# Optimization experiments

Measured on AMD Instinct MI355X. Metric: run time of the kernel, lower is better.

Reference implementation:

```python
import jax, jax.numpy as jnp
import numpy as np
import math

PS = 16            # patch size for SigmaPredictor
HID = 8            # hidden_dim
SCALE = HID ** -0.5
SIGMA_CAP = 6.0    # BoundedSoftplus threshold
EPS_S = 1e-6       # BoundedSoftplus eps


def setup_inputs() -> dict:
    key = jax.random.key(0)
    ks = jax.random.split(key, 10)
    B, C, H, W = 2, 1, 384, 384
    d_in = C * PS * PS  # 256
    r = lambda k_, sh: jax.random.normal(k_, sh, dtype=jnp.float32) * 0.1
    z = lambda sh: jnp.zeros(sh, dtype=jnp.float32)
    return {
        "x": jax.random.uniform(ks[0], (B, C, H, W), dtype=jnp.float32),
        "Wq": r(ks[1], (d_in, HID)), "bq": z((HID,)),
        "Wk": r(ks[2], (d_in, HID)), "bk": z((HID,)),
        "Wv": r(ks[3], (d_in, HID)), "bv": z((HID,)),
        "Wsq": r(ks[4], (HID, HID)), "bsq": z((HID,)),
        "Wsk": r(ks[5], (HID, HID)), "bsk": z((HID,)),
        "Wsv": r(ks[6], (HID, HID)), "bsv": z((HID,)),
        "ln_g": jnp.ones((HID,), jnp.float32), "ln_b": z((HID,)),
        "Wp": r(ks[7], (HID, 3)),
        # bias ~4 -> sigmas ~4 -> kernel size k=13 (production-scale support)
        "bp": jnp.full((3,), 4.0, dtype=jnp.float32),
    }


def _attn(q, k, v):
    a = jax.nn.softmax(jnp.einsum('bnd,bmd->bnm', q, k) * SCALE, axis=-1)
    return jnp.einsum('bnm,bmd->bnd', a, v)


def _predict_sigmas(x, Wq, bq, Wk, bk, Wv, bv, Wsq, bsq, Wsk, bsk, Wsv, bsv, ln_g, ln_b, Wp, bp):
    b, c, h, w = x.shape
    Hp, Wn = h // PS, w // PS
    # unfold into non-overlapping patches: [B, Hp*Wn, C*PS*PS]
    pat = x.reshape(b, c, Hp, PS, Wn, PS).transpose(0, 2, 4, 1, 3, 5).reshape(b, Hp * Wn, c * PS * PS)
    feats = _attn(pat @ Wq + bq, pat @ Wk + bk, pat @ Wv + bv)
    o = _attn(feats @ Wsq + bsq, feats @ Wsk + bsk, feats @ Wsv + bsv)
    mu = o.mean(-1, keepdims=True)
    var = ((o - mu) ** 2).mean(-1, keepdims=True)
    o = (o - mu) / jnp.sqrt(var + 1e-5) * ln_g + ln_b
    s = jnp.minimum(jax.nn.softplus(o @ Wp + bp), SIGMA_CAP) + EPS_S  # BoundedSoftplus
    s = s.reshape(b, Hp, Wn, 3)
    # nearest-neighbor upsample to full resolution: [B, H, W, 3]
    return jnp.repeat(jnp.repeat(s, PS, axis=1), PS, axis=2)


def _bilateral(x, s, k):
    b, c, h, w = x.shape
    sx, sy, sr = s[..., 0], s[..., 1], s[..., 2]
    half = k // 2
    xp = jnp.pad(x, ((0, 0), (0, 0), (half, half), (half, half)))
    # [B, C, H, W, k*k], dy-major to match torch unfold/meshgrid ordering
    patches = jnp.stack([xp[:, :, dy:dy + h, dx:dx + w]
                         for dy in range(k) for dx in range(k)], axis=-1)
    coords = jnp.arange(-half, half + 1, dtype=jnp.float32)
    yy, xx = jnp.meshgrid(coords, coords, indexing='ij')
    xx2 = (xx ** 2).reshape(-1)
    yy2 = (yy ** 2).reshape(-1)
    # spatial kernel [B, H, W, k*k]
    sp = jnp.exp(-xx2 / (2 * sx[..., None] ** 2) - yy2 / (2 * sy[..., None] ** 2))
    # range kernel (C == 1 branch) [B, C, H, W, k*k]
    rg = jnp.exp(-(x[..., None] - patches) ** 2 / (2 * sr[:, None, :, :, None] ** 2))
    comb = sp[:, None] * rg
    norm = comb / (comb.sum(-1, keepdims=True) + 1e-8)
    return (patches * norm).sum(-1)


def reference(x, Wq, bq, Wk, bk, Wv, bv, Wsq, bsq, Wsk, bsk, Wsv, bsv, ln_g, ln_b, Wp, bp):
    s = _predict_sigmas(x, Wq, bq, Wk, bk, Wv, bv, Wsq, bsq, Wsk, bsk, Wsv, bsv, ln_g, ln_b, Wp, bp)
    # data-dependent kernel size, computed eagerly (matches torch .item())
    m = float(jnp.maximum(s[..., 0].max(), s[..., 1].max()))
    k = int(2 * math.ceil(m + 1))
    if k % 2 == 0:
        k += 1
    return _bilateral(x, s, k)
```

## Files before the change

### kernel.cpp

```cpp
#include <hip/hip_runtime.h>

#define N_TOK 576
#define HP    24
#define PS    16
#define IMG   384
#define ATTN_SCALE 0.35355339059327373f

__global__ __launch_bounds__(256) void k_qkv1(
    const float* __restrict__ x,
    const float* __restrict__ Wq, const float* __restrict__ bq,
    const float* __restrict__ Wk, const float* __restrict__ bk,
    const float* __restrict__ Wv, const float* __restrict__ bv,
    float* __restrict__ q1, float* __restrict__ k1, float* __restrict__ v1,
    int* __restrict__ smax)
{
    const int blk = blockIdx.x;
    const int b  = blk / N_TOK;
    const int n  = blk % N_TOK;
    const int py = n / HP, px = n % HP;
    const int t  = threadIdx.x;
    const int iy = t >> 4, ix = t & 15;

    if (blk == 0 && t == 0) smax[0] = 0;

    const float pv = x[b*IMG*IMG + (py*PS + iy)*IMG + (px*PS + ix)];

    float acc[24];
#pragma unroll
    for (int h = 0; h < 8; ++h) {
        acc[h]      = pv * Wq[t*8 + h];
        acc[8 + h]  = pv * Wk[t*8 + h];
        acc[16 + h] = pv * Wv[t*8 + h];
    }
#pragma unroll
    for (int off = 32; off > 0; off >>= 1) {
#pragma unroll
        for (int j = 0; j < 24; ++j)
            acc[j] += __shfl_down(acc[j], off);
    }
    __shared__ float red[4][24];
    const int lane = t & 63, w = t >> 6;
    if (lane == 0) {
#pragma unroll
        for (int j = 0; j < 24; ++j) red[w][j] = acc[j];
    }
    __syncthreads();
    if (t < 24) {
        float s = red[0][t] + red[1][t] + red[2][t] + red[3][t];
        const int h = t & 7, mat = t >> 3;
        const float* bias = (mat == 0) ? bq : (mat == 1) ? bk : bv;
        float* dst = (mat == 0) ? q1 : (mat == 1) ? k1 : v1;
        dst[(b*N_TOK + n)*8 + h] = s + bias[h];
    }
}

__device__ __forceinline__ void attn_core(
    const float* __restrict__ qp, const float* __restrict__ kb,
    const float* __restrict__ vb, int lane, float f[8], float* ssum_out)
{
    const float4 qa = *(const float4*)(qp);
    const float4 qb_ = *(const float4*)(qp + 4);
    float qv[8] = {qa.x, qa.y, qa.z, qa.w, qb_.x, qb_.y, qb_.z, qb_.w};

    float sc[9], mx = -1e30f;
#pragma unroll
    for (int ch = 0; ch < 9; ++ch) {
        const float* kp = kb + (ch*64 + lane)*8;
        const float4 ka = *(const float4*)(kp);
        const float4 kb2 = *(const float4*)(kp + 4);
        float d = qv[0]*ka.x + qv[1]*ka.y + qv[2]*ka.z + qv[3]*ka.w
                + qv[4]*kb2.x + qv[5]*kb2.y + qv[6]*kb2.z + qv[7]*kb2.w;
        d *= ATTN_SCALE;
        sc[ch] = d;
        mx = fmaxf(mx, d);
    }
#pragma unroll
    for (int off = 32; off > 0; off >>= 1) mx = fmaxf(mx, __shfl_xor(mx, off));

    float ssum = 0.f, o[8];
#pragma unroll
    for (int h = 0; h < 8; ++h) o[h] = 0.f;
#pragma unroll
    for (int ch = 0; ch < 9; ++ch) {
        const float p = __expf(sc[ch] - mx);
        ssum += p;
        const float* vp = vb + (ch*64 + lane)*8;
        const float4 va = *(const float4*)(vp);
        const float4 vb2 = *(const float4*)(vp + 4);
        o[0] += p*va.x;  o[1] += p*va.y;  o[2] += p*va.z;  o[3] += p*va.w;
        o[4] += p*vb2.x; o[5] += p*vb2.y; o[6] += p*vb2.z; o[7] += p*vb2.w;
    }
#pragma unroll
    for (int off = 32; off > 0; off >>= 1) {
        ssum += __shfl_xor(ssum, off);
#pragma unroll
        for (int h = 0; h < 8; ++h) o[h] += __shfl_xor(o[h], off);
    }
    const float inv = 1.f/ssum;
#pragma unroll
    for (int h = 0; h < 8; ++h) f[h] = o[h]*inv;
    *ssum_out = ssum;
}

__global__ __launch_bounds__(256) void k_attn1(
    const float* __restrict__ q1, const float* __restrict__ k1, const float* __restrict__ v1,
    const float* __restrict__ Wsq, const float* __restrict__ bsq,
    const float* __restrict__ Wsk, const float* __restrict__ bsk,
    const float* __restrict__ Wsv, const float* __restrict__ bsv,
    float* __restrict__ q2, float* __restrict__ k2, float* __restrict__ v2)
{
    const int lane = threadIdx.x & 63;
    const int wv   = threadIdx.x >> 6;
    const int tok  = blockIdx.x*4 + wv;
    const int b    = tok / N_TOK;

    float f[8], ssum;
    attn_core(q1 + tok*8, k1 + b*N_TOK*8, v1 + b*N_TOK*8, lane, f, &ssum);

    if (lane < 24) {
        const int mat = lane >> 3, h = lane & 7;
        const float* Wm = (mat==0)?Wsq:(mat==1)?Wsk:Wsv;
        const float* bm = (mat==0)?bsq:(mat==1)?bsk:bsv;
        float s = bm[h];
#pragma unroll
        for (int j = 0; j < 8; ++j) s += f[j]*Wm[j*8 + h];
        float* dst = (mat==0)?q2:(mat==1)?k2:v2;
        dst[tok*8 + h] = s;
    }
}

__global__ __launch_bounds__(256) void k_attn2(
    const float* __restrict__ q2, const float* __restrict__ k2, const float* __restrict__ v2,
    const float* __restrict__ ln_g, const float* __restrict__ ln_b,
    const float* __restrict__ Wp,   const float* __restrict__ bp,
    float* __restrict__ sig, int* __restrict__ smax)
{
    const int lane = threadIdx.x & 63;
    const int wv   = threadIdx.x >> 6;
    const int tok  = blockIdx.x*4 + wv;
    const int b    = tok / N_TOK;

    float f[8], ssum;
    attn_core(q2 + tok*8, k2 + b*N_TOK*8, v2 + b*N_TOK*8, lane, f, &ssum);

    if (lane == 0) {
        float mu = 0.f;
#pragma unroll
        for (int h = 0; h < 8; ++h) mu += f[h];
        mu *= 0.125f;
        float var = 0.f;
#pragma unroll
        for (int h = 0; h < 8; ++h) { const float d = f[h]-mu; var += d*d; }
        var *= 0.125f;
        const float rinv = rsqrtf(var + 1e-5f);
        float on[8];
#pragma unroll
        for (int h = 0; h < 8; ++h)
            on[h] = (f[h]-mu)*rinv*ln_g[h] + ln_b[h];
        float sv[3];
#pragma unroll
        for (int c = 0; c < 3; ++c) {
            float z = bp[c];
#pragma unroll
            for (int j = 0; j < 8; ++j) z += on[j]*Wp[j*3 + c];
            const float sp = (z > 20.f) ? z : log1pf(__expf(z));
            sv[c] = fminf(sp, 6.0f) + 1e-6f;
            sig[tok*3 + c] = sv[c];
        }
        atomicMax(smax, __float_as_int(fmaxf(sv[0], sv[1])));
    }
}

template<int HALF>
__device__ __forceinline__ float bilat_core(
    const float* __restrict__ tile, int tx, int ty,
    float ax, float ay, float ar)
{
    constexpr int K = 2*HALF + 1;
    const float c = tile[(ty+HALF)*40 + (tx+HALF)];

    float ex[K];
#pragma unroll
    for (int d = 0; d < K; ++d) {
        const float fd = (float)(d - HALF);
        ex[d] = ax*fd*fd;
    }

    float num = 0.f, den = 0.f;
#pragma unroll
    for (int dy = 0; dy < K; ++dy) {
        const float fy = (float)(dy - HALF);
        const float ey = ay*fy*fy;
        const float* row = &tile[(ty+dy)*40 + tx];
#pragma unroll
        for (int dx = 0; dx < K; ++dx) {
            const float p = row[dx];
            const float d = c - p;
            const float w = __expf(ey + ex[dx] + ar*d*d);
            den += w;
            num += w*p;
        }
    }
    return num/(den + 1e-8f);
}

__global__ __launch_bounds__(256) void k_bilat(
    const float* __restrict__ x, const float* __restrict__ sig,
    const int* __restrict__ smaxi, float* __restrict__ out)
{
    __shared__ float tile[32*40];
    const int blk = blockIdx.x;
    const int b  = blk / N_TOK;
    const int n  = blk % N_TOK;
    const int py = n / HP, px = n % HP;
    const int tx = threadIdx.x & 15, ty = threadIdx.x >> 4;

    const float m = __int_as_float(smaxi[0]);
    int half = (int)ceilf(m + 1.0f);
    half = (half < 1) ? 1 : (half > 8) ? 8 : half;

    const float sx = sig[blk*3 + 0];
    const float sy = sig[blk*3 + 1];
    const float sr = sig[blk*3 + 2];

    const int tilew = PS + 2*half;
    const float* xb = x + b*IMG*IMG;
    for (int yy = ty; yy < tilew; yy += 16) {
        const int gy = py*PS + yy - half;
        for (int xx = tx; xx < tilew; xx += 16) {
            const int gx = px*PS + xx - half;
            float v = 0.f;
            if ((unsigned)gy < IMG && (unsigned)gx < IMG)
                v = xb[gy*IMG + gx];
            tile[yy*40 + xx] = v;
        }
    }
    __syncthreads();

    const float ax = -0.5f/(sx*sx);
    const float ay = -0.5f/(sy*sy);
    const float ar = -0.5f/(sr*sr);

    float r;
    switch (half) {
        case 1: r = bilat_core<1>(tile, tx, ty, ax, ay, ar); break;
        case 2: r = bilat_core<2>(tile, tx, ty, ax, ay, ar); break;
        case 3: r = bilat_core<3>(tile, tx, ty, ax, ay, ar); break;
        case 4: r = bilat_core<4>(tile, tx, ty, ax, ay, ar); break;
        case 5: r = bilat_core<5>(tile, tx, ty, ax, ay, ar); break;
        case 6: r = bilat_core<6>(tile, tx, ty, ax, ay, ar); break;
        case 7: r = bilat_core<7>(tile, tx, ty, ax, ay, ar); break;
        default: r = bilat_core<8>(tile, tx, ty, ax, ay, ar); break;
    }
    out[b*IMG*IMG + (py*PS + ty)*IMG + (px*PS + tx)] = r;
}

extern "C" void kernel_launch(void* const* d_in, const int* in_sizes, int n_in,
                              void* d_out, int out_size, void* d_ws, size_t ws_size,
                              hipStream_t stream)
{
    const float* x    = (const float*)d_in[0];
    const float* Wq   = (const float*)d_in[1];
    const float* bq   = (const float*)d_in[2];
    const float* Wk   = (const float*)d_in[3];
    const float* bk   = (const float*)d_in[4];
    const float* Wv   = (const float*)d_in[5];
    const float* bv   = (const float*)d_in[6];
    const float* Wsq  = (const float*)d_in[7];
    const float* bsq  = (const float*)d_in[8];
    const float* Wsk  = (const float*)d_in[9];
    const float* bsk  = (const float*)d_in[10];
    const float* Wsv  = (const float*)d_in[11];
    const float* bsv  = (const float*)d_in[12];
    const float* ln_g = (const float*)d_in[13];
    const float* ln_b = (const float*)d_in[14];
    const float* Wp   = (const float*)d_in[15];
    const float* bp   = (const float*)d_in[16];

    float* W  = (float*)d_ws;
    float* q1 = W;
    float* k1 = W +  9216;
    float* v1 = W + 18432;
    float* q2 = W + 27648;
    float* k2 = W + 36864;
    float* v2 = W + 46080;
    float* sg = W + 55296;
    int* smax = (int*)(W + 58752);

    k_qkv1<<<2*N_TOK, 256, 0, stream>>>(x, Wq, bq, Wk, bk, Wv, bv, q1, k1, v1, smax);
    k_attn1<<<2*N_TOK/4, 256, 0, stream>>>(q1, k1, v1, Wsq, bsq, Wsk, bsk, Wsv, bsv,
                                           q2, k2, v2);
    k_attn2<<<2*N_TOK/4, 256, 0, stream>>>(q2, k2, v2, ln_g, ln_b, Wp, bp, sg, smax);
    k_bilat<<<2*N_TOK, 256, 0, stream>>>(x, sg, smax, (float*)d_out);
}
```

Before: 146.7 us.

## Fuse all four stages into one cooperative persistent kernel with grid syncs

Replaces the four separate launches (qkv projection, two attention stages, bilateral filter) with a single cooperative kernel of 256 persistent blocks that loops over tasks and separates stages with grid.sync(). The goal is to remove per-launch overhead and inter-kernel gaps, which dominate for such small stages. The cost is that each stage now runs on only 256 blocks with launch_bounds(256,1), so the heavy bilateral stage gets less parallelism per wave. Grid-wide barriers also add their own latency. The original four-kernel path is kept as a fallback if the cooperative launch fails.

```diff
diff --git a/kernel.cpp b/kernel.cpp
--- a/kernel.cpp
+++ b/kernel.cpp
@@ -1,62 +1,18 @@
 #include <hip/hip_runtime.h>
+#include <hip/hip_cooperative_groups.h>
+
+namespace cg = cooperative_groups;
 
 #define N_TOK 576
 #define HP    24
 #define PS    16
 #define IMG   384
+#define GRID  256
 #define ATTN_SCALE 0.35355339059327373f
-
-__global__ __launch_bounds__(256) void k_qkv1(
-    const float* __restrict__ x,
-    const float* __restrict__ Wq, const float* __restrict__ bq,
-    const float* __restrict__ Wk, const float* __restrict__ bk,
-    const float* __restrict__ Wv, const float* __restrict__ bv,
-    float* __restrict__ q1, float* __restrict__ k1, float* __restrict__ v1,
-    int* __restrict__ smax)
-{
-    const int blk = blockIdx.x;
-    const int b  = blk / N_TOK;
-    const int n  = blk % N_TOK;
-    const int py = n / HP, px = n % HP;
-    const int t  = threadIdx.x;
-    const int iy = t >> 4, ix = t & 15;
-
-    if (blk == 0 && t == 0) smax[0] = 0;
-
-    const float pv = x[b*IMG*IMG + (py*PS + iy)*IMG + (px*PS + ix)];
-
-    float acc[24];
-#pragma unroll
-    for (int h = 0; h < 8; ++h) {
-        acc[h]      = pv * Wq[t*8 + h];
-        acc[8 + h]  = pv * Wk[t*8 + h];
-        acc[16 + h] = pv * Wv[t*8 + h];
-    }
-#pragma unroll
-    for (int off = 32; off > 0; off >>= 1) {
-#pragma unroll
-        for (int j = 0; j < 24; ++j)
-            acc[j] += __shfl_down(acc[j], off);
-    }
-    __shared__ float red[4][24];
-    const int lane = t & 63, w = t >> 6;
-    if (lane == 0) {
-#pragma unroll
-        for (int j = 0; j < 24; ++j) red[w][j] = acc[j];
-    }
-    __syncthreads();
-    if (t < 24) {
-        float s = red[0][t] + red[1][t] + red[2][t] + red[3][t];
-        const int h = t & 7, mat = t >> 3;
-        const float* bias = (mat == 0) ? bq : (mat == 1) ? bk : bv;
-        float* dst = (mat == 0) ? q1 : (mat == 1) ? k1 : v1;
-        dst[(b*N_TOK + n)*8 + h] = s + bias[h];
-    }
-}
 
 __device__ __forceinline__ void attn_core(
     const float* __restrict__ qp, const float* __restrict__ kb,
-    const float* __restrict__ vb, int lane, float f[8], float* ssum_out)
+    const float* __restrict__ vb, int lane, float f[8])
 {
     const float4 qa = *(const float4*)(qp);
     const float4 qb_ = *(const float4*)(qp + 4);
@@ -99,24 +55,64 @@
     const float inv = 1.f/ssum;
 #pragma unroll
     for (int h = 0; h < 8; ++h) f[h] = o[h]*inv;
-    *ssum_out = ssum;
-}
-
-__global__ __launch_bounds__(256) void k_attn1(
+}
+
+__device__ __forceinline__ void qkv1_body(
+    int task, int t,
+    const float* __restrict__ x,
+    const float* __restrict__ Wq, const float* __restrict__ bq,
+    const float* __restrict__ Wk, const float* __restrict__ bk,
+    const float* __restrict__ Wv, const float* __restrict__ bv,
+    float* __restrict__ q1, float* __restrict__ k1, float* __restrict__ v1,
+    float red[4][24])
+{
+    const int b  = task / N_TOK;
+    const int n  = task % N_TOK;
+    const int py = n / HP, px = n % HP;
+    const int iy = t >> 4, ix = t & 15;
+    const int lane = t & 63, wv = t >> 6;
+
+    const float pv = x[b*IMG*IMG + (py*PS + iy)*IMG + (px*PS + ix)];
+
+    float acc[24];
+#pragma unroll
+    for (int h = 0; h < 8; ++h) {
+        acc[h]      = pv * Wq[t*8 + h];
+        acc[8 + h]  = pv * Wk[t*8 + h];
+        acc[16 + h] = pv * Wv[t*8 + h];
+    }
+#pragma unroll
+    for (int off = 32; off > 0; off >>= 1) {
+#pragma unroll
+        for (int j = 0; j < 24; ++j)
+            acc[j] += __shfl_down(acc[j], off);
+    }
+    if (lane == 0) {
+#pragma unroll
+        for (int j = 0; j < 24; ++j) red[wv][j] = acc[j];
+    }
+    __syncthreads();
+    if (t < 24) {
+        float s = red[0][t] + red[1][t] + red[2][t] + red[3][t];
+        const int h = t & 7, mat = t >> 3;
+        const float* bias = (mat == 0) ? bq : (mat == 1) ? bk : bv;
+        float* dst = (mat == 0) ? q1 : (mat == 1) ? k1 : v1;
+        dst[task*8 + h] = s + bias[h];
+    }
+    __syncthreads();
+}
+
+__device__ __forceinline__ void attn1_body(
+    int tok, int lane,
     const float* __restrict__ q1, const float* __restrict__ k1, const float* __restrict__ v1,
     const float* __restrict__ Wsq, const float* __restrict__ bsq,
     const float* __restrict__ Wsk, const float* __restrict__ bsk,
     const float* __restrict__ Wsv, const float* __restrict__ bsv,
     float* __restrict__ q2, float* __restrict__ k2, float* __restrict__ v2)
 {
-    const int lane = threadIdx.x & 63;
-    const int wv   = threadIdx.x >> 6;
-    const int tok  = blockIdx.x*4 + wv;
-    const int b    = tok / N_TOK;
-
-    float f[8], ssum;
-    attn_core(q1 + tok*8, k1 + b*N_TOK*8, v1 + b*N_TOK*8, lane, f, &ssum);
-
+    const int b = tok / N_TOK;
+    float f[8];
+    attn_core(q1 + tok*8, k1 + b*N_TOK*8, v1 + b*N_TOK*8, lane, f);
     if (lane < 24) {
         const int mat = lane >> 3, h = lane & 7;
         const float* Wm = (mat==0)?Wsq:(mat==1)?Wsk:Wsv;
@@ -129,20 +125,16 @@
     }
 }
 
-__global__ __launch_bounds__(256) void k_attn2(
+__device__ __forceinline__ void attn2_body(
+    int tok, int lane,
     const float* __restrict__ q2, const float* __restrict__ k2, const float* __restrict__ v2,
     const float* __restrict__ ln_g, const float* __restrict__ ln_b,
     const float* __restrict__ Wp,   const float* __restrict__ bp,
     float* __restrict__ sig, int* __restrict__ smax)
 {
-    const int lane = threadIdx.x & 63;
-    const int wv   = threadIdx.x >> 6;
-    const int tok  = blockIdx.x*4 + wv;
-    const int b    = tok / N_TOK;
-
-    float f[8], ssum;
-    attn_core(q2 + tok*8, k2 + b*N_TOK*8, v2 + b*N_TOK*8, lane, f, &ssum);
-
+    const int b = tok / N_TOK;
+    float f[8];
+    attn_core(q2 + tok*8, k2 + b*N_TOK*8, v2 + b*N_TOK*8, lane, f);
     if (lane == 0) {
         float mu = 0.f;
 #pragma unroll
@@ -204,26 +196,21 @@
     return num/(den + 1e-8f);
 }
 
-__global__ __launch_bounds__(256) void k_bilat(
+__device__ __forceinline__ void bilat_body(
+    int task, int t, int half,
     const float* __restrict__ x, const float* __restrict__ sig,
-    const int* __restrict__ smaxi, float* __restrict__ out)
-{
-    __shared__ float tile[32*40];
-    const int blk = blockIdx.x;
-    const int b  = blk / N_TOK;
-    const int n  = blk % N_TOK;
+    float* __restrict__ out, float* __restrict__ tile)
+{
+    const int b  = task / N_TOK;
+    const int n  = task % N_TOK;
     const int py = n / HP, px = n % HP;
-    const int tx = threadIdx.x & 15, ty = threadIdx.x >> 4;
-
-    const float m = __int_as_float(smaxi[0]);
-    int half = (int)ceilf(m + 1.0f);
-    half = (half < 1) ? 1 : (half > 8) ? 8 : half;
-
-    const float sx = sig[blk*3 + 0];
-    const float sy = sig[blk*3 + 1];
-    const float sr = sig[blk*3 + 2];
-
+    const int tx = t & 15, ty = t >> 4;
     const int tilew = PS + 2*half;
+
+    const float sx = sig[task*3 + 0];
+    const float sy = sig[task*3 + 1];
+    const float sr = sig[task*3 + 2];
+
     const float* xb = x + b*IMG*IMG;
     for (int yy = ty; yy < tilew; yy += 16) {
         const int gy = py*PS + yy - half;
@@ -253,6 +240,103 @@
         default: r = bilat_core<8>(tile, tx, ty, ax, ay, ar); break;
     }
     out[b*IMG*IMG + (py*PS + ty)*IMG + (px*PS + tx)] = r;
+    __syncthreads();
+}
+
+__device__ __forceinline__ int half_from_smax(const int* smax)
+{
+    const float m = __int_as_float(smax[0]);
+    int half = (int)ceilf(m + 1.0f);
+    return (half < 1) ? 1 : (half > 8) ? 8 : half;
+}
+
+__global__ __launch_bounds__(256, 1) void k_fused(
+    const float* __restrict__ x,
+    const float* __restrict__ Wq,  const float* __restrict__ bq,
+    const float* __restrict__ Wk,  const float* __restrict__ bk,
+    const float* __restrict__ Wv,  const float* __restrict__ bv,
+    const float* __restrict__ Wsq, const float* __restrict__ bsq,
+    const float* __restrict__ Wsk, const float* __restrict__ bsk,
+    const float* __restrict__ Wsv, const float* __restrict__ bsv,
+    const float* __restrict__ ln_g, const float* __restrict__ ln_b,
+    const float* __restrict__ Wp,   const float* __restrict__ bp,
+    float* __restrict__ q1, float* __restrict__ k1, float* __restrict__ v1,
+    float* __restrict__ q2, float* __restrict__ k2, float* __restrict__ v2,
+    float* __restrict__ sig, int* __restrict__ smax,
+    float* __restrict__ out)
+{
+    cg::grid_group grid = cg::this_grid();
+
+    const int t    = threadIdx.x;
+    const int lane = t & 63;
+    const int wv   = t >> 6;
+
+    __shared__ float red[4][24];
+    __shared__ float tile[32*40];
+
+    if (blockIdx.x == 0 && t == 0) smax[0] = 0;
+
+    for (int task = blockIdx.x; task < 2*N_TOK; task += GRID)
+        qkv1_body(task, t, x, Wq, bq, Wk, bk, Wv, bv, q1, k1, v1, red);
+    grid.sync();
+
+    for (int tok = blockIdx.x*4 + wv; tok < 2*N_TOK; tok += GRID*4)
+        attn1_body(tok, lane, q1, k1, v1, Wsq, bsq, Wsk, bsk, Wsv, bsv,
+                   q2, k2, v2);
+    grid.sync();
+
+    for (int tok = blockIdx.x*4 + wv; tok < 2*N_TOK; tok += GRID*4)
+        attn2_body(tok, lane, q2, k2, v2, ln_g, ln_b, Wp, bp, sig, smax);
+    grid.sync();
+
+    const int half = half_from_smax(smax);
+    for (int task = blockIdx.x; task < 2*N_TOK; task += GRID)
+        bilat_body(task, t, half, x, sig, out, tile);
+}
+
+__global__ __launch_bounds__(256) void k_qkv1(
+    const float* __restrict__ x,
+    const float* __restrict__ Wq, const float* __restrict__ bq,
+    const float* __restrict__ Wk, const float* __restrict__ bk,
+    const float* __restrict__ Wv, const float* __restrict__ bv,
+    float* __restrict__ q1, float* __restrict__ k1, float* __restrict__ v1,
+    int* __restrict__ smax)
+{
+    __shared__ float red[4][24];
+    if (blockIdx.x == 0 && threadIdx.x == 0) smax[0] = 0;
+    qkv1_body(blockIdx.x, threadIdx.x, x, Wq, bq, Wk, bk, Wv, bv,
+              q1, k1, v1, red);
+}
+
+__global__ __launch_bounds__(256) void k_attn1(
+    const float* __restrict__ q1, const float* __restrict__ k1, const float* __restrict__ v1,
+    const float* __restrict__ Wsq, const float* __restrict__ bsq,
+    const float* __restrict__ Wsk, const float* __restrict__ bsk,
+    const float* __restrict__ Wsv, const float* __restrict__ bsv,
+    float* __restrict__ q2, float* __restrict__ k2, float* __restrict__ v2)
+{
+    const int tok = blockIdx.x*4 + (threadIdx.x >> 6);
+    attn1_body(tok, threadIdx.x & 63, q1, k1, v1, Wsq, bsq, Wsk, bsk,
+               Wsv, bsv, q2, k2, v2);
+}
+
+__global__ __launch_bounds__(256) void k_attn2(
+    const float* __restrict__ q2, const float* __restrict__ k2, const float* __restrict__ v2,
+    const float* __restrict__ ln_g, const float* __restrict__ ln_b,
+    const float* __restrict__ Wp,   const float* __restrict__ bp,
+    float* __restrict__ sig, int* __restrict__ smax)
+{
+    const int tok = blockIdx.x*4 + (threadIdx.x >> 6);
+    attn2_body(tok, threadIdx.x & 63, q2, k2, v2, ln_g, ln_b, Wp, bp, sig, smax);
+}
+
+__global__ __launch_bounds__(256) void k_bilat(
+    const float* __restrict__ x, const float* __restrict__ sig,
+    const int* __restrict__ smax, float* __restrict__ out)
+{
+    __shared__ float tile[32*40];
+    const int half = half_from_smax(smax);
+    bilat_body(blockIdx.x, threadIdx.x, half, x, sig, out, tile);
 }
 
 extern "C" void kernel_launch(void* const* d_in, const int* in_sizes, int n_in,
@@ -286,10 +370,29 @@
     float* v2 = W + 46080;
     float* sg = W + 55296;
     int* smax = (int*)(W + 58752);
-
-    k_qkv1<<<2*N_TOK, 256, 0, stream>>>(x, Wq, bq, Wk, bk, Wv, bv, q1, k1, v1, smax);
-    k_attn1<<<2*N_TOK/4, 256, 0, stream>>>(q1, k1, v1, Wsq, bsq, Wsk, bsk, Wsv, bsv,
-                                           q2, k2, v2);
-    k_attn2<<<2*N_TOK/4, 256, 0, stream>>>(q2, k2, v2, ln_g, ln_b, Wp, bp, sg, smax);
-    k_bilat<<<2*N_TOK, 256, 0, stream>>>(x, sg, smax, (float*)d_out);
-}
+    float* out = (float*)d_out;
+
+    void* args[] = {
+        (void*)&x,
+        (void*)&Wq,  (void*)&bq,  (void*)&Wk,  (void*)&bk,
+        (void*)&Wv,  (void*)&bv,
+        (void*)&Wsq, (void*)&bsq, (void*)&Wsk, (void*)&bsk,
+        (void*)&Wsv, (void*)&bsv,
+        (void*)&ln_g, (void*)&ln_b, (void*)&Wp, (void*)&bp,
+        (void*)&q1, (void*)&k1, (void*)&v1,
+        (void*)&q2, (void*)&k2, (void*)&v2,
+        (void*)&sg, (void*)&smax, (void*)&out
+    };
+    hipError_t err = hipLaunchCooperativeKernel((const void*)k_fused,
+                                                dim3(GRID), dim3(256),
+                                                args, 0, stream);
+    if (err != hipSuccess) {
+        k_qkv1<<<2*N_TOK, 256, 0, stream>>>(x, Wq, bq, Wk, bk, Wv, bv,
+                                            q1, k1, v1, smax);
+        k_attn1<<<2*N_TOK/4, 256, 0, stream>>>(q1, k1, v1, Wsq, bsq, Wsk, bsk,
+                                               Wsv, bsv, q2, k2, v2);
+        k_attn2<<<2*N_TOK/4, 256, 0, stream>>>(q2, k2, v2, ln_g, ln_b, Wp, bp,
+                                               sg, smax);
+        k_bilat<<<2*N_TOK, 256, 0, stream>>>(x, sg, smax, out);
+    }
+}
```

Result: slower. 247.2 us (+68.5%).
